# Kernel optimization log

Measured on AMD Instinct MI355X. Metric: run time of the kernel, lower is better.

Reference implementation:

```python
import jax, jax.numpy as jnp
import numpy as np
from jax import lax

T, N, E = 8192, 33, 64
D_IN, D_H, D_LSTM, N_CLS = 3, 64, 128, 5


def _lin(k, out_d, in_d):
    return jax.random.normal(k, (out_d, in_d), jnp.float32) / np.sqrt(in_d)


def setup_inputs() -> dict:
    key = jax.random.key(0)
    ks = jax.random.split(key, 16)
    x = jax.random.normal(ks[0], (T, N, D_IN), jnp.float32)
    edge_src = jax.random.randint(ks[1], (E,), 0, N)
    edge_dst = jax.random.randint(ks[2], (E,), 0, N)
    return {
        "x": x,
        "edge_src": edge_src,
        "edge_dst": edge_dst,
        "W_rel1": _lin(ks[3], D_H, D_IN),
        "b_rel1": jnp.zeros((D_H,), jnp.float32),
        "W_root1": _lin(ks[4], D_H, D_IN),
        "W_rel2": _lin(ks[5], D_H, D_H),
        "b_rel2": jnp.zeros((D_H,), jnp.float32),
        "W_root2": _lin(ks[6], D_H, D_H),
        "W_ih": _lin(ks[7], 4 * D_LSTM, D_H),
        "W_hh": _lin(ks[8], 4 * D_LSTM, D_LSTM),
        "b_ih": jnp.zeros((4 * D_LSTM,), jnp.float32),
        "b_hh": jnp.zeros((4 * D_LSTM,), jnp.float32),
        "W_fc": _lin(ks[9], N_CLS, D_LSTM),
        "b_fc": jnp.zeros((N_CLS,), jnp.float32),
    }


def graph_conv(x, src, dst, W_rel, b_rel, W_root):
    # PyG GraphConv (aggr='add'): lin_rel(scatter_add(x[src] -> dst)) + lin_root(x)
    msg = x[:, src, :]                              # [T, E, d]
    agg = jnp.zeros_like(x).at[:, dst, :].add(msg)  # [T, N, d]
    return agg @ W_rel.T + b_rel + x @ W_root.T     # [T, N, out]


def lstm_last_hidden(seq, W_ih, W_hh, b_ih, b_hh):
    # seq: [T, D_H]; torch gate order i, f, g, o
    def step(carry, xt):
        h, c = carry
        gates = xt @ W_ih.T + h @ W_hh.T + b_ih + b_hh  # [4*D_LSTM]
        i, f, g, o = jnp.split(gates, 4)
        c = jax.nn.sigmoid(f) * c + jax.nn.sigmoid(i) * jnp.tanh(g)
        h = jax.nn.sigmoid(o) * jnp.tanh(c)
        return (h, c), None
    init = (jnp.zeros((D_LSTM,), seq.dtype), jnp.zeros((D_LSTM,), seq.dtype))
    (hT, _), _ = lax.scan(step, init, seq)
    return hT


def reference(x, edge_src, edge_dst, W_rel1, b_rel1, W_root1, W_rel2, b_rel2,
              W_root2, W_ih, W_hh, b_ih, b_hh, W_fc, b_fc):
    h = graph_conv(x, edge_src, edge_dst, W_rel1, b_rel1, W_root1)  # [T,N,64]
    h = graph_conv(h, edge_src, edge_dst, W_rel2, b_rel2, W_root2)  # [T,N,64]
    h = jax.nn.relu(h)
    seq = h.mean(axis=1)                                            # global_mean_pool per frame -> [T,64]
    hT = lstm_last_hidden(seq, W_ih, W_hh, b_ih, b_hh)              # [128]
    return (hT @ W_fc.T + b_fc)[None, :]                            # [1, 5]
```

## Files before the change

### kernel.cpp

```cpp
#include <hip/hip_runtime.h>
#include <hip/hip_fp16.h>

#define T_LEN 8192
#define N_NODES 33
#define N_EDGES 64
#define DIM_IN 3
#define D_H 64
#define D_LSTM 128
#define N_CLS 5
#define TB 4

typedef float v2f __attribute__((ext_vector_type(2)));
typedef float v4f __attribute__((ext_vector_type(4)));

__global__ __launch_bounds__(64, 2) void gnn_proj_kernel(
    const float* __restrict__ x,
    const int*   __restrict__ esrc,
    const int*   __restrict__ edst,
    const float* __restrict__ W_rel1,
    const float* __restrict__ b_rel1,
    const float* __restrict__ W_root1,
    const float* __restrict__ W_rel2,
    const float* __restrict__ b_rel2,
    const float* __restrict__ W_root2,
    const float* __restrict__ W_ih,
    const float* __restrict__ b_ih,
    const float* __restrict__ b_hh,
    float* __restrict__ A)
{
    const int t0 = blockIdx.x * TB;
    const int j  = threadIdx.x;

    __shared__ __align__(16) float x_s[N_NODES][DIM_IN];
    __shared__ __align__(16) float agg1[N_NODES][DIM_IN];
    __shared__ __align__(16) float h1[N_NODES][D_H];
    __shared__ __align__(16) float agg2[N_NODES][D_H];
    __shared__ __align__(16) float seq_s[TB][D_H];
    __shared__ int es[N_EDGES], ed[N_EDGES];

    es[j] = esrc[j];
    ed[j] = edst[j];

    const float wr1_0 = W_rel1[j*3+0], wr1_1 = W_rel1[j*3+1], wr1_2 = W_rel1[j*3+2];
    const float wt1_0 = W_root1[j*3+0], wt1_1 = W_root1[j*3+1], wt1_2 = W_root1[j*3+2];
    const float br1 = b_rel1[j];
    const float br2 = b_rel2[j];

    float wr2[D_H], wt2[D_H];
    #pragma unroll
    for (int k = 0; k < D_H; ++k) {
        wr2[k] = W_rel2[j*D_H + k];
        wt2[k] = W_root2[j*D_H + k];
    }

    for (int tt = 0; tt < TB; ++tt) {
        const int t = t0 + tt;
        __syncthreads();

        const float* xt = x + (size_t)t * (N_NODES * DIM_IN);
        for (int i = j; i < N_NODES * DIM_IN; i += 64) x_s[0][i] = xt[i];
        __syncthreads();

        if (j < N_NODES) {
            float a0 = 0.f, a1 = 0.f, a2 = 0.f;
            for (int e = 0; e < N_EDGES; ++e) {
                if (ed[e] == j) {
                    a0 += x_s[es[e]][0];
                    a1 += x_s[es[e]][1];
                    a2 += x_s[es[e]][2];
                }
            }
            agg1[j][0] = a0; agg1[j][1] = a1; agg1[j][2] = a2;
        }
        __syncthreads();

        for (int n = 0; n < N_NODES; ++n) {
            float v = br1
                + agg1[n][0]*wr1_0 + agg1[n][1]*wr1_1 + agg1[n][2]*wr1_2
                + x_s[n][0]*wt1_0  + x_s[n][1]*wt1_1  + x_s[n][2]*wt1_2;
            h1[n][j]  = v;
            agg2[n][j] = 0.f;
        }
        __syncthreads();

        for (int e = 0; e < N_EDGES; ++e) {
            agg2[ed[e]][j] += h1[es[e]][j];
        }
        __syncthreads();

        float seqv = 0.f;
        for (int n = 0; n < N_NODES; ++n) {
            const float4* ag4 = (const float4*)agg2[n];
            const float4* h4  = (const float4*)h1[n];
            float acc0 = br2, acc1 = 0.f, acc2 = 0.f, acc3 = 0.f;
            #pragma unroll
            for (int k4 = 0; k4 < D_H/4; ++k4) {
                float4 av = ag4[k4];
                float4 hv = h4[k4];
                acc0 += av.x * wr2[4*k4+0] + hv.x * wt2[4*k4+0];
                acc1 += av.y * wr2[4*k4+1] + hv.y * wt2[4*k4+1];
                acc2 += av.z * wr2[4*k4+2] + hv.z * wt2[4*k4+2];
                acc3 += av.w * wr2[4*k4+3] + hv.w * wt2[4*k4+3];
            }
            float acc = (acc0 + acc1) + (acc2 + acc3);
            seqv += fmaxf(acc, 0.f);
        }
        seq_s[tt][j] = seqv * (1.0f / 33.0f);
    }
    __syncthreads();

    #pragma unroll
    for (int m = 0; m < 8; ++m) {
        const int o = m * 64 + j;
        const float bias = b_ih[o] + b_hh[o];
        const float4* w4 = (const float4*)(W_ih + (size_t)o * D_H);
        float acc[TB];
        #pragma unroll
        for (int tt = 0; tt < TB; ++tt) acc[tt] = bias;
        #pragma unroll
        for (int k4 = 0; k4 < D_H/4; ++k4) {
            float4 wv = w4[k4];
            #pragma unroll
            for (int tt = 0; tt < TB; ++tt) {
                const float4* s4 = (const float4*)seq_s[tt];
                float4 sv = s4[k4];
                acc[tt] += sv.x*wv.x + sv.y*wv.y + sv.z*wv.z + sv.w*wv.w;
            }
        }
        #pragma unroll
        for (int tt = 0; tt < TB; ++tt) {
            A[((size_t)(t0 + tt) * 128 + (o & 127)) * 4 + (o >> 7)] = acc[tt];
        }
    }
}


#define CVTPK(D,S0,S1) \
  "v_cvt_f16_f32 v190, v" #S0 "\n\t" \
  "v_cvt_f16_f32 v191, v" #S1 "\n\t" \
  "v_and_b32 v190, 0xffff, v190\n\t" \
  "v_lshlrev_b32 v191, 16, v191\n\t" \
  "v_or_b32 v" #D ", v190, v191\n\t"

#define ROWPACK(D0,D1,D2,D3,D4,D5,D6,D7,D8,D9,D10,D11,D12,D13,D14,D15) \
  CVTPK(D0,128,129) CVTPK(D1,130,131) CVTPK(D2,132,133) CVTPK(D3,134,135) \
  CVTPK(D4,136,137) CVTPK(D5,138,139) CVTPK(D6,140,141) CVTPK(D7,142,143) \
  CVTPK(D8,144,145) CVTPK(D9,146,147) CVTPK(D10,148,149) CVTPK(D11,150,151) \
  CVTPK(D12,152,153) CVTPK(D13,154,155) CVTPK(D14,156,157) CVTPK(D15,158,159)

#define FRAGLOAD(WA) \
  "global_load_dwordx4 v[128:131], %[" #WA "], off\n\t" \
  "global_load_dwordx4 v[132:135], %[" #WA "], off offset:16\n\t" \
  "global_load_dwordx4 v[136:139], %[" #WA "], off offset:128\n\t" \
  "global_load_dwordx4 v[140:143], %[" #WA "], off offset:144\n\t" \
  "global_load_dwordx4 v[144:147], %[" #WA "], off offset:256\n\t" \
  "global_load_dwordx4 v[148:151], %[" #WA "], off offset:272\n\t" \
  "global_load_dwordx4 v[152:155], %[" #WA "], off offset:384\n\t" \
  "global_load_dwordx4 v[156:159], %[" #WA "], off offset:400\n\t" \
  "s_waitcnt vmcnt(0)\n\t"

#define HALF(P0,P3, PC0,PC1,PC2,PC3, R0,R1,R2,R3, WOFF) \
  "ds_read_b128 v[64:67], %[rb] offset:" #R0 "\n\t" \
  "ds_read_b128 v[68:71], %[rb] offset:" #R1 "\n\t" \
  "ds_read_b128 v[72:75], %[rb] offset:" #R2 "\n\t" \
  "ds_read_b128 v[76:79], %[rb] offset:" #R3 "\n\t" \
  "v_add_u32 v189, s80, %[at]\n\t" \
  "global_load_dwordx4 v[" #P0 ":" #P3 "], v189, %[ab]\n\t" \
  "s_add_u32 s80, s80, 2048\n\t" \
  "s_cmp_lg_u32 s80, 0x1000000\n\t" \
  "s_cselect_b32 s80, s80, 0\n\t" \
  "s_waitcnt lgkmcnt(0)\n\t" \
   \
  "v_mfma_f32_16x16x32_f16 v[80:83], v[0:3],   v[64:67], v[164:167]\n\t" \
  "v_mfma_f32_16x16x32_f16 v[84:87], v[16:19], v[64:67], v[164:167]\n\t" \
  "v_mfma_f32_16x16x32_f16 v[88:91], v[32:35], v[64:67], v[164:167]\n\t" \
  "v_mfma_f32_16x16x32_f16 v[92:95], v[48:51], v[64:67], v[164:167]\n\t" \
  "v_mfma_f32_16x16x32_f16 v[80:83], v[4:7],   v[68:71], v[80:83]\n\t" \
  "v_mfma_f32_16x16x32_f16 v[84:87], v[20:23], v[68:71], v[84:87]\n\t" \
  "v_mfma_f32_16x16x32_f16 v[88:91], v[36:39], v[68:71], v[88:91]\n\t" \
  "v_mfma_f32_16x16x32_f16 v[92:95], v[52:55], v[68:71], v[92:95]\n\t" \
  "v_mfma_f32_16x16x32_f16 v[80:83], v[8:11],  v[72:75], v[80:83]\n\t" \
  "v_mfma_f32_16x16x32_f16 v[84:87], v[24:27], v[72:75], v[84:87]\n\t" \
  "v_mfma_f32_16x16x32_f16 v[88:91], v[40:43], v[72:75], v[88:91]\n\t" \
  "v_mfma_f32_16x16x32_f16 v[92:95], v[56:59], v[72:75], v[92:95]\n\t" \
  "v_mfma_f32_16x16x32_f16 v[80:83], v[12:15], v[76:79], v[80:83]\n\t" \
  "v_mfma_f32_16x16x32_f16 v[84:87], v[28:31], v[76:79], v[84:87]\n\t" \
  "v_mfma_f32_16x16x32_f16 v[88:91], v[44:47], v[76:79], v[88:91]\n\t" \
  "v_mfma_f32_16x16x32_f16 v[92:95], v[60:63], v[76:79], v[92:95]\n\t" \
  "s_nop 7\n\t" \
  "s_nop 7\n\t" \
   \
  "v_cndmask_b32 v184, v80, v82, %[sb1]\n\t" \
  "v_cndmask_b32 v185, v81, v83, %[sb1]\n\t" \
  "v_cndmask_b32 v176, v184, v185, %[sb0]\n\t" \
  "v_cndmask_b32 v184, v84, v86, %[sb1]\n\t" \
  "v_cndmask_b32 v185, v85, v87, %[sb1]\n\t" \
  "v_cndmask_b32 v177, v184, v185, %[sb0]\n\t" \
  "v_cndmask_b32 v184, v88, v90, %[sb1]\n\t" \
  "v_cndmask_b32 v185, v89, v91, %[sb1]\n\t" \
  "v_cndmask_b32 v178, v184, v185, %[sb0]\n\t" \
  "v_cndmask_b32 v184, v92, v94, %[sb1]\n\t" \
  "v_cndmask_b32 v185, v93, v95, %[sb1]\n\t" \
  "v_cndmask_b32 v179, v184, v185, %[sb0]\n\t" \
   \
  "s_waitcnt vmcnt(1)\n\t" \
  "v_add_f32 v176, v176, v" #PC0 "\n\t" \
  "v_add_f32 v177, v177, v" #PC1 "\n\t" \
  "v_add_f32 v178, v178, v" #PC2 "\n\t" \
  "v_add_f32 v179, v179, v" #PC3 "\n\t" \
   \
  "v_mul_f32 v180, s87, v176\n\t" \
  "v_mul_f32 v181, s87, v177\n\t" \
  "v_mul_f32 v182, s87, v179\n\t" \
  "v_mul_f32 v183, s88, v178\n\t" \
  "v_exp_f32 v180, v180\n\t" \
  "v_exp_f32 v181, v181\n\t" \
  "v_exp_f32 v182, v182\n\t" \
  "v_exp_f32 v183, v183\n\t" \
  "v_add_f32 v180, 1.0, v180\n\t" \
  "v_add_f32 v181, 1.0, v181\n\t" \
  "v_add_f32 v182, 1.0, v182\n\t" \
  "v_add_f32 v183, 1.0, v183\n\t" \
  "v_rcp_f32 v183, v183\n\t" \
  "v_rcp_f32 v180, v180\n\t" \
  "v_rcp_f32 v181, v181\n\t" \
  "v_rcp_f32 v182, v182\n\t" \
  "v_add_f32 v183, v183, v183\n\t" \
  "v_add_f32 v183, -1.0, v183\n\t" \
  "v_mul_f32 v184, v180, v183\n\t" \
  "v_fma_f32 v190, v181, v190, v184\n\t" \
  "v_mul_f32 v185, s88, v190\n\t" \
  "v_exp_f32 v185, v185\n\t" \
  "s_nop 1\n\t" \
  "v_add_f32 v185, 1.0, v185\n\t" \
  "v_rcp_f32 v185, v185\n\t" \
  "s_nop 1\n\t" \
  "v_fma_f32 v185, v185, 2.0, -1.0\n\t" \
  "v_mul_f32 v188, v182, v185\n\t" \
  "v_cvt_f16_f32 v188, v188\n\t" \
   \
  "s_and_saveexec_b64 s[84:85], s[82:83]\n\t" \
  "ds_write_b16 %[wr], v188 offset:" #WOFF "\n\t" \
  "s_mov_b64 exec, s[84:85]\n\t" \
  "s_waitcnt lgkmcnt(0)\n\t" \
  "s_barrier\n\t"

__global__ __launch_bounds__(512, 2)
__attribute__((amdgpu_waves_per_eu(2, 2)))
void lstm_kernel(
    const float* __restrict__ A,
    const float* __restrict__ W_hh,
    const float* __restrict__ W_fc,
    const float* __restrict__ b_fc,
    float* __restrict__ out)
{
    const int tid  = threadIdx.x;
    const int lane = tid & 63;
    const int wave = tid >> 6;
    const int q0   = wave * 16;
    const int row  = lane & 15;
    const int kb8  = (lane >> 4) * 8;
    const int u    = q0 + 4 * (lane >> 4) + (lane & 3);

    __shared__ __align__(16) float h_s[2][64];

    if (tid < 128) ((float*)h_s)[tid] = 0.f;
    __syncthreads();

    const unsigned long long wai = (unsigned long long)(uintptr_t)(W_hh + (size_t)(q0 + row)        * D_LSTM + kb8);
    const unsigned long long waf = (unsigned long long)(uintptr_t)(W_hh + (size_t)(128 + q0 + row)  * D_LSTM + kb8);
    const unsigned long long wag = (unsigned long long)(uintptr_t)(W_hh + (size_t)(256 + q0 + row)  * D_LSTM + kb8);
    const unsigned long long wao = (unsigned long long)(uintptr_t)(W_hh + (size_t)(384 + q0 + row)  * D_LSTM + kb8);
    const unsigned int atid = (unsigned int)(u * 16);
    const unsigned int lds0 = (unsigned int)(uintptr_t)&h_s[0][0];
    const unsigned int rb   = lds0 + (unsigned int)((lane >> 4) * 16);
    const unsigned int wr   = lds0 + (unsigned int)(u * 2);
    const unsigned long long wm  = __ballot((lane & 12) == 0);
    const unsigned long long sb0 = __ballot(lane & 1);
    const unsigned long long sb1 = __ballot(lane & 2);

    asm volatile(
        "s_mov_b32 s80, 2048\n\t"
        "s_mov_b32 s86, 4096\n\t"
        "s_mov_b32 s87, 0xBFB8AA3B\n\t"
        "s_mov_b32 s88, 0xC038AA3B\n\t"
        "s_mov_b64 s[82:83], %[wm]\n\t"
        FRAGLOAD(wai)
        ROWPACK(0,1,2,3,4,5,6,7,8,9,10,11,12,13,14,15)
        FRAGLOAD(waf)
        ROWPACK(16,17,18,19,20,21,22,23,24,25,26,27,28,29,30,31)
        FRAGLOAD(wag)
        ROWPACK(32,33,34,35,36,37,38,39,40,41,42,43,44,45,46,47)
        FRAGLOAD(wao)
        ROWPACK(48,49,50,51,52,53,54,55,56,57,58,59,60,61,62,63)
        "v_mov_b32 v164, 0\n\t"
        "v_mov_b32 v165, 0\n\t"
        "v_mov_b32 v166, 0\n\t"
        "v_mov_b32 v167, 0\n\t"
        "global_load_dwordx4 v[168:171], %[at], %[ab]\n\t"
        "s_waitcnt vmcnt(0)\n\t"
        "v_mov_b32 v190, 0\n\t"
        "1:\n\t"
        HALF(172,175, 168,169,170,171, 0,64,128,192, 256)
        HALF(168,171, 172,173,174,175, 256,320,384,448, 0)
        "s_sub_u32 s86, s86, 1\n\t"
        "s_cmp_lg_u32 s86, 0\n\t"
        "s_cbranch_scc1 1b\n\t"
        :
        : [wai]"v"(wai), [waf]"v"(waf), [wag]"v"(wag), [wao]"v"(wao),
          [ab]"s"(A), [at]"v"(atid), [rb]"v"(rb), [wr]"v"(wr), [wm]"s"(wm),
          [sb0]"s"(sb0), [sb1]"s"(sb1)
        : "v0","v1","v2","v3","v4","v5","v6","v7","v8","v9",
          "v10","v11","v12","v13","v14","v15","v16","v17","v18","v19",
          "v20","v21","v22","v23","v24","v25","v26","v27","v28","v29",
          "v30","v31","v32","v33","v34","v35","v36","v37","v38","v39",
          "v40","v41","v42","v43","v44","v45","v46","v47","v48","v49",
          "v50","v51","v52","v53","v54","v55","v56","v57","v58","v59",
          "v60","v61","v62","v63","v64","v65","v66","v67","v68","v69",
          "v70","v71","v72","v73","v74","v75","v76","v77","v78","v79",
          "v80","v81","v82","v83","v84","v85","v86","v87","v88","v89",
          "v90","v91","v92","v93","v94","v95","v96","v97","v98","v99",
          "v100","v101","v102","v103","v104","v105","v106","v107","v108","v109",
          "v110","v111","v112","v113","v114","v115","v116","v117","v118","v119",
          "v120","v121","v122","v123","v124","v125","v126","v127","v128","v129",
          "v130","v131","v132","v133","v134","v135","v136","v137","v138","v139",
          "v140","v141","v142","v143","v144","v145","v146","v147","v148","v149",
          "v150","v151","v152","v153","v154","v155","v156","v157","v158","v159",
          "v160","v161","v162","v163","v164","v165","v166","v167","v168","v169",
          "v170","v171","v172","v173","v174","v175","v176","v177","v178","v179",
          "v180","v181","v182","v183","v184","v185","v186","v187","v188","v189",
          "v190","v191",
          "s80","s81","s82","s83","s84","s85","s86","s87","s88",
          "scc","memory"
    );

    __syncthreads();

    if (tid < N_CLS) {
        const __half* hh = (const __half*)&h_s[0][0];
        float acc = b_fc[tid];
        #pragma unroll
        for (int k = 0; k < D_LSTM; ++k) {
            acc += __half2float(hh[k]) * W_fc[tid * D_LSTM + k];
        }
        out[tid] = acc;
    }
}

extern "C" void kernel_launch(void* const* d_in, const int* in_sizes, int n_in,
                              void* d_out, int out_size, void* d_ws, size_t ws_size,
                              hipStream_t stream) {
    const float* x       = (const float*)d_in[0];
    const int*   esrc    = (const int*)  d_in[1];
    const int*   edst    = (const int*)  d_in[2];
    const float* W_rel1  = (const float*)d_in[3];
    const float* b_rel1  = (const float*)d_in[4];
    const float* W_root1 = (const float*)d_in[5];
    const float* W_rel2  = (const float*)d_in[6];
    const float* b_rel2  = (const float*)d_in[7];
    const float* W_root2 = (const float*)d_in[8];
    const float* W_ih    = (const float*)d_in[9];
    const float* W_hh    = (const float*)d_in[10];
    const float* b_ih    = (const float*)d_in[11];
    const float* b_hh    = (const float*)d_in[12];
    const float* W_fc    = (const float*)d_in[13];
    const float* b_fc    = (const float*)d_in[14];

    float* out = (float*)d_out;
    float* A   = (float*)d_ws;

    gnn_proj_kernel<<<T_LEN / TB, 64, 0, stream>>>(
        x, esrc, edst, W_rel1, b_rel1, W_root1,
        W_rel2, b_rel2, W_root2, W_ih, b_ih, b_hh, A);

    lstm_kernel<<<1, 512, 0, stream>>>(A, W_hh, W_fc, b_fc, out);
}
```

Measured before the change: 3.876 ms.

## Halve LSTM workgroup to four waves, each computing two hidden-unit groups

The sequential LSTM kernel now runs with 256 threads (4 waves) instead of 512. Each wave holds twice as many W_hh fragments in registers and issues 32 MFMAs per half-step, computing two hidden units per lane. The aim is to cut barrier and synchronisation cost per timestep by involving fewer waves. The trade-offs are a longer per-wave critical path, since each wave does twice the MFMA and transcendental work, and much higher VGPR use.

```diff
diff --git a/kernel.cpp b/kernel.cpp
--- a/kernel.cpp
+++ b/kernel.cpp
@@ -136,117 +136,176 @@
 
 
 #define CVTPK(D,S0,S1) \
-  "v_cvt_f16_f32 v190, v" #S0 "\n\t" \
-  "v_cvt_f16_f32 v191, v" #S1 "\n\t" \
-  "v_and_b32 v190, 0xffff, v190\n\t" \
-  "v_lshlrev_b32 v191, 16, v191\n\t" \
-  "v_or_b32 v" #D ", v190, v191\n\t"
+  "v_cvt_f16_f32 v204, v" #S0 "\n\t" \
+  "v_cvt_f16_f32 v205, v" #S1 "\n\t" \
+  "v_and_b32 v204, 0xffff, v204\n\t" \
+  "v_lshlrev_b32 v205, 16, v205\n\t" \
+  "v_or_b32 v" #D ", v204, v205\n\t"
 
 #define ROWPACK(D0,D1,D2,D3,D4,D5,D6,D7,D8,D9,D10,D11,D12,D13,D14,D15) \
-  CVTPK(D0,128,129) CVTPK(D1,130,131) CVTPK(D2,132,133) CVTPK(D3,134,135) \
-  CVTPK(D4,136,137) CVTPK(D5,138,139) CVTPK(D6,140,141) CVTPK(D7,142,143) \
-  CVTPK(D8,144,145) CVTPK(D9,146,147) CVTPK(D10,148,149) CVTPK(D11,150,151) \
-  CVTPK(D12,152,153) CVTPK(D13,154,155) CVTPK(D14,156,157) CVTPK(D15,158,159)
-
-#define FRAGLOAD(WA) \
-  "global_load_dwordx4 v[128:131], %[" #WA "], off\n\t" \
-  "global_load_dwordx4 v[132:135], %[" #WA "], off offset:16\n\t" \
-  "global_load_dwordx4 v[136:139], %[" #WA "], off offset:128\n\t" \
-  "global_load_dwordx4 v[140:143], %[" #WA "], off offset:144\n\t" \
-  "global_load_dwordx4 v[144:147], %[" #WA "], off offset:256\n\t" \
-  "global_load_dwordx4 v[148:151], %[" #WA "], off offset:272\n\t" \
-  "global_load_dwordx4 v[152:155], %[" #WA "], off offset:384\n\t" \
-  "global_load_dwordx4 v[156:159], %[" #WA "], off offset:400\n\t" \
+  CVTPK(D0,144,145) CVTPK(D1,146,147) CVTPK(D2,148,149) CVTPK(D3,150,151) \
+  CVTPK(D4,152,153) CVTPK(D5,154,155) CVTPK(D6,156,157) CVTPK(D7,158,159) \
+  CVTPK(D8,160,161) CVTPK(D9,162,163) CVTPK(D10,164,165) CVTPK(D11,166,167) \
+  CVTPK(D12,168,169) CVTPK(D13,170,171) CVTPK(D14,172,173) CVTPK(D15,174,175)
+
+#define FRAGLOAD(VOFF) \
+  "global_load_dwordx4 v[144:147], " VOFF ", %[whh]\n\t" \
+  "global_load_dwordx4 v[148:151], " VOFF ", %[whh] offset:16\n\t" \
+  "global_load_dwordx4 v[152:155], " VOFF ", %[whh] offset:128\n\t" \
+  "global_load_dwordx4 v[156:159], " VOFF ", %[whh] offset:144\n\t" \
+  "global_load_dwordx4 v[160:163], " VOFF ", %[whh] offset:256\n\t" \
+  "global_load_dwordx4 v[164:167], " VOFF ", %[whh] offset:272\n\t" \
+  "global_load_dwordx4 v[168:171], " VOFF ", %[whh] offset:384\n\t" \
+  "global_load_dwordx4 v[172:175], " VOFF ", %[whh] offset:400\n\t" \
   "s_waitcnt vmcnt(0)\n\t"
 
-#define HALF(P0,P3, PC0,PC1,PC2,PC3, R0,R1,R2,R3, WOFF) \
-  "ds_read_b128 v[64:67], %[rb] offset:" #R0 "\n\t" \
-  "ds_read_b128 v[68:71], %[rb] offset:" #R1 "\n\t" \
-  "ds_read_b128 v[72:75], %[rb] offset:" #R2 "\n\t" \
-  "ds_read_b128 v[76:79], %[rb] offset:" #R3 "\n\t" \
-  "v_add_u32 v189, s80, %[at]\n\t" \
-  "global_load_dwordx4 v[" #P0 ":" #P3 "], v189, %[ab]\n\t" \
+#define HALF(P0,P3,P4,P7, PC0,PC1,PC2,PC3,PC4,PC5,PC6,PC7, R0,R1,R2,R3, W1,W2) \
+  "ds_read_b128 v[128:131], %[rb] offset:" #R0 "\n\t" \
+  "ds_read_b128 v[132:135], %[rb] offset:" #R1 "\n\t" \
+  "ds_read_b128 v[136:139], %[rb] offset:" #R2 "\n\t" \
+  "ds_read_b128 v[140:143], %[rb] offset:" #R3 "\n\t" \
+  "v_add_u32 v232, s80, %[at]\n\t" \
+  "global_load_dwordx4 v[" #P0 ":" #P3 "], v232, %[ab]\n\t" \
+  "global_load_dwordx4 v[" #P4 ":" #P7 "], v232, %[ab] offset:256\n\t" \
   "s_add_u32 s80, s80, 2048\n\t" \
   "s_cmp_lg_u32 s80, 0x1000000\n\t" \
   "s_cselect_b32 s80, s80, 0\n\t" \
   "s_waitcnt lgkmcnt(0)\n\t" \
    \
-  "v_mfma_f32_16x16x32_f16 v[80:83], v[0:3],   v[64:67], v[164:167]\n\t" \
-  "v_mfma_f32_16x16x32_f16 v[84:87], v[16:19], v[64:67], v[164:167]\n\t" \
-  "v_mfma_f32_16x16x32_f16 v[88:91], v[32:35], v[64:67], v[164:167]\n\t" \
-  "v_mfma_f32_16x16x32_f16 v[92:95], v[48:51], v[64:67], v[164:167]\n\t" \
-  "v_mfma_f32_16x16x32_f16 v[80:83], v[4:7],   v[68:71], v[80:83]\n\t" \
-  "v_mfma_f32_16x16x32_f16 v[84:87], v[20:23], v[68:71], v[84:87]\n\t" \
-  "v_mfma_f32_16x16x32_f16 v[88:91], v[36:39], v[68:71], v[88:91]\n\t" \
-  "v_mfma_f32_16x16x32_f16 v[92:95], v[52:55], v[68:71], v[92:95]\n\t" \
-  "v_mfma_f32_16x16x32_f16 v[80:83], v[8:11],  v[72:75], v[80:83]\n\t" \
-  "v_mfma_f32_16x16x32_f16 v[84:87], v[24:27], v[72:75], v[84:87]\n\t" \
-  "v_mfma_f32_16x16x32_f16 v[88:91], v[40:43], v[72:75], v[88:91]\n\t" \
-  "v_mfma_f32_16x16x32_f16 v[92:95], v[56:59], v[72:75], v[92:95]\n\t" \
-  "v_mfma_f32_16x16x32_f16 v[80:83], v[12:15], v[76:79], v[80:83]\n\t" \
-  "v_mfma_f32_16x16x32_f16 v[84:87], v[28:31], v[76:79], v[84:87]\n\t" \
-  "v_mfma_f32_16x16x32_f16 v[88:91], v[44:47], v[76:79], v[88:91]\n\t" \
-  "v_mfma_f32_16x16x32_f16 v[92:95], v[60:63], v[76:79], v[92:95]\n\t" \
+  "v_mfma_f32_16x16x32_f16 v[144:147], v[0:3],     v[128:131], v[200:203]\n\t" \
+  "v_mfma_f32_16x16x32_f16 v[148:151], v[16:19],   v[128:131], v[200:203]\n\t" \
+  "v_mfma_f32_16x16x32_f16 v[152:155], v[32:35],   v[128:131], v[200:203]\n\t" \
+  "v_mfma_f32_16x16x32_f16 v[156:159], v[48:51],   v[128:131], v[200:203]\n\t" \
+  "v_mfma_f32_16x16x32_f16 v[160:163], v[64:67],   v[128:131], v[200:203]\n\t" \
+  "v_mfma_f32_16x16x32_f16 v[164:167], v[80:83],   v[128:131], v[200:203]\n\t" \
+  "v_mfma_f32_16x16x32_f16 v[168:171], v[96:99],   v[128:131], v[200:203]\n\t" \
+  "v_mfma_f32_16x16x32_f16 v[172:175], v[112:115], v[128:131], v[200:203]\n\t" \
+  "v_mfma_f32_16x16x32_f16 v[144:147], v[4:7],     v[132:135], v[144:147]\n\t" \
+  "v_mfma_f32_16x16x32_f16 v[148:151], v[20:23],   v[132:135], v[148:151]\n\t" \
+  "v_mfma_f32_16x16x32_f16 v[152:155], v[36:39],   v[132:135], v[152:155]\n\t" \
+  "v_mfma_f32_16x16x32_f16 v[156:159], v[52:55],   v[132:135], v[156:159]\n\t" \
+  "v_mfma_f32_16x16x32_f16 v[160:163], v[68:71],   v[132:135], v[160:163]\n\t" \
+  "v_mfma_f32_16x16x32_f16 v[164:167], v[84:87],   v[132:135], v[164:167]\n\t" \
+  "v_mfma_f32_16x16x32_f16 v[168:171], v[100:103], v[132:135], v[168:171]\n\t" \
+  "v_mfma_f32_16x16x32_f16 v[172:175], v[116:119], v[132:135], v[172:175]\n\t" \
+  "v_mfma_f32_16x16x32_f16 v[144:147], v[8:11],    v[136:139], v[144:147]\n\t" \
+  "v_mfma_f32_16x16x32_f16 v[148:151], v[24:27],   v[136:139], v[148:151]\n\t" \
+  "v_mfma_f32_16x16x32_f16 v[152:155], v[40:43],   v[136:139], v[152:155]\n\t" \
+  "v_mfma_f32_16x16x32_f16 v[156:159], v[56:59],   v[136:139], v[156:159]\n\t" \
+  "v_mfma_f32_16x16x32_f16 v[160:163], v[72:75],   v[136:139], v[160:163]\n\t" \
+  "v_mfma_f32_16x16x32_f16 v[164:167], v[88:91],   v[136:139], v[164:167]\n\t" \
+  "v_mfma_f32_16x16x32_f16 v[168:171], v[104:107], v[136:139], v[168:171]\n\t" \
+  "v_mfma_f32_16x16x32_f16 v[172:175], v[120:123], v[136:139], v[172:175]\n\t" \
+  "v_mfma_f32_16x16x32_f16 v[144:147], v[12:15],   v[140:143], v[144:147]\n\t" \
+  "v_mfma_f32_16x16x32_f16 v[148:151], v[28:31],   v[140:143], v[148:151]\n\t" \
+  "v_mfma_f32_16x16x32_f16 v[152:155], v[44:47],   v[140:143], v[152:155]\n\t" \
+  "v_mfma_f32_16x16x32_f16 v[156:159], v[60:63],   v[140:143], v[156:159]\n\t" \
+  "v_mfma_f32_16x16x32_f16 v[160:163], v[76:79],   v[140:143], v[160:163]\n\t" \
+  "v_mfma_f32_16x16x32_f16 v[164:167], v[92:95],   v[140:143], v[164:167]\n\t" \
+  "v_mfma_f32_16x16x32_f16 v[168:171], v[108:111], v[140:143], v[168:171]\n\t" \
+  "v_mfma_f32_16x16x32_f16 v[172:175], v[124:127], v[140:143], v[172:175]\n\t" \
   "s_nop 7\n\t" \
   "s_nop 7\n\t" \
    \
-  "v_cndmask_b32 v184, v80, v82, %[sb1]\n\t" \
-  "v_cndmask_b32 v185, v81, v83, %[sb1]\n\t" \
-  "v_cndmask_b32 v176, v184, v185, %[sb0]\n\t" \
-  "v_cndmask_b32 v184, v84, v86, %[sb1]\n\t" \
-  "v_cndmask_b32 v185, v85, v87, %[sb1]\n\t" \
-  "v_cndmask_b32 v177, v184, v185, %[sb0]\n\t" \
-  "v_cndmask_b32 v184, v88, v90, %[sb1]\n\t" \
-  "v_cndmask_b32 v185, v89, v91, %[sb1]\n\t" \
-  "v_cndmask_b32 v178, v184, v185, %[sb0]\n\t" \
-  "v_cndmask_b32 v184, v92, v94, %[sb1]\n\t" \
-  "v_cndmask_b32 v185, v93, v95, %[sb1]\n\t" \
-  "v_cndmask_b32 v179, v184, v185, %[sb0]\n\t" \
+  "v_cndmask_b32 v204, v144, v146, %[sb1]\n\t" \
+  "v_cndmask_b32 v205, v145, v147, %[sb1]\n\t" \
+  "v_cndmask_b32 v208, v204, v205, %[sb0]\n\t" \
+  "v_cndmask_b32 v204, v148, v150, %[sb1]\n\t" \
+  "v_cndmask_b32 v205, v149, v151, %[sb1]\n\t" \
+  "v_cndmask_b32 v209, v204, v205, %[sb0]\n\t" \
+  "v_cndmask_b32 v204, v152, v154, %[sb1]\n\t" \
+  "v_cndmask_b32 v205, v153, v155, %[sb1]\n\t" \
+  "v_cndmask_b32 v210, v204, v205, %[sb0]\n\t" \
+  "v_cndmask_b32 v204, v156, v158, %[sb1]\n\t" \
+  "v_cndmask_b32 v205, v157, v159, %[sb1]\n\t" \
+  "v_cndmask_b32 v211, v204, v205, %[sb0]\n\t" \
+  "v_cndmask_b32 v204, v160, v162, %[sb1]\n\t" \
+  "v_cndmask_b32 v205, v161, v163, %[sb1]\n\t" \
+  "v_cndmask_b32 v212, v204, v205, %[sb0]\n\t" \
+  "v_cndmask_b32 v204, v164, v166, %[sb1]\n\t" \
+  "v_cndmask_b32 v205, v165, v167, %[sb1]\n\t" \
+  "v_cndmask_b32 v213, v204, v205, %[sb0]\n\t" \
+  "v_cndmask_b32 v204, v168, v170, %[sb1]\n\t" \
+  "v_cndmask_b32 v205, v169, v171, %[sb1]\n\t" \
+  "v_cndmask_b32 v214, v204, v205, %[sb0]\n\t" \
+  "v_cndmask_b32 v204, v172, v174, %[sb1]\n\t" \
+  "v_cndmask_b32 v205, v173, v175, %[sb1]\n\t" \
+  "v_cndmask_b32 v215, v204, v205, %[sb0]\n\t" \
    \
-  "s_waitcnt vmcnt(1)\n\t" \
-  "v_add_f32 v176, v176, v" #PC0 "\n\t" \
-  "v_add_f32 v177, v177, v" #PC1 "\n\t" \
-  "v_add_f32 v178, v178, v" #PC2 "\n\t" \
-  "v_add_f32 v179, v179, v" #PC3 "\n\t" \
+  "s_waitcnt vmcnt(2)\n\t" \
+  "v_add_f32 v208, v208, v" #PC0 "\n\t" \
+  "v_add_f32 v209, v209, v" #PC1 "\n\t" \
+  "v_add_f32 v210, v210, v" #PC2 "\n\t" \
+  "v_add_f32 v211, v211, v" #PC3 "\n\t" \
+  "v_add_f32 v212, v212, v" #PC4 "\n\t" \
+  "v_add_f32 v213, v213, v" #PC5 "\n\t" \
+  "v_add_f32 v214, v214, v" #PC6 "\n\t" \
+  "v_add_f32 v215, v215, v" #PC7 "\n\t" \
    \
-  "v_mul_f32 v180, s87, v176\n\t" \
-  "v_mul_f32 v181, s87, v177\n\t" \
-  "v_mul_f32 v182, s87, v179\n\t" \
-  "v_mul_f32 v183, s88, v178\n\t" \
-  "v_exp_f32 v180, v180\n\t" \
-  "v_exp_f32 v181, v181\n\t" \
-  "v_exp_f32 v182, v182\n\t" \
-  "v_exp_f32 v183, v183\n\t" \
-  "v_add_f32 v180, 1.0, v180\n\t" \
-  "v_add_f32 v181, 1.0, v181\n\t" \
-  "v_add_f32 v182, 1.0, v182\n\t" \
-  "v_add_f32 v183, 1.0, v183\n\t" \
-  "v_rcp_f32 v183, v183\n\t" \
-  "v_rcp_f32 v180, v180\n\t" \
-  "v_rcp_f32 v181, v181\n\t" \
-  "v_rcp_f32 v182, v182\n\t" \
-  "v_add_f32 v183, v183, v183\n\t" \
-  "v_add_f32 v183, -1.0, v183\n\t" \
-  "v_mul_f32 v184, v180, v183\n\t" \
-  "v_fma_f32 v190, v181, v190, v184\n\t" \
-  "v_mul_f32 v185, s88, v190\n\t" \
-  "v_exp_f32 v185, v185\n\t" \
+  "v_mul_f32 v216, s87, v208\n\t" \
+  "v_mul_f32 v217, s87, v209\n\t" \
+  "v_mul_f32 v218, s88, v210\n\t" \
+  "v_mul_f32 v219, s87, v211\n\t" \
+  "v_mul_f32 v220, s87, v212\n\t" \
+  "v_mul_f32 v221, s87, v213\n\t" \
+  "v_mul_f32 v222, s88, v214\n\t" \
+  "v_mul_f32 v223, s87, v215\n\t" \
+  "v_exp_f32 v216, v216\n\t" \
+  "v_exp_f32 v217, v217\n\t" \
+  "v_exp_f32 v218, v218\n\t" \
+  "v_exp_f32 v219, v219\n\t" \
+  "v_exp_f32 v220, v220\n\t" \
+  "v_exp_f32 v221, v221\n\t" \
+  "v_exp_f32 v222, v222\n\t" \
+  "v_exp_f32 v223, v223\n\t" \
+  "v_add_f32 v216, 1.0, v216\n\t" \
+  "v_add_f32 v217, 1.0, v217\n\t" \
+  "v_add_f32 v218, 1.0, v218\n\t" \
+  "v_add_f32 v219, 1.0, v219\n\t" \
+  "v_add_f32 v220, 1.0, v220\n\t" \
+  "v_add_f32 v221, 1.0, v221\n\t" \
+  "v_add_f32 v222, 1.0, v222\n\t" \
+  "v_add_f32 v223, 1.0, v223\n\t" \
+  "v_rcp_f32 v218, v218\n\t" \
+  "v_rcp_f32 v222, v222\n\t" \
+  "v_rcp_f32 v216, v216\n\t" \
+  "v_rcp_f32 v217, v217\n\t" \
+  "v_rcp_f32 v219, v219\n\t" \
+  "v_rcp_f32 v220, v220\n\t" \
+  "v_rcp_f32 v221, v221\n\t" \
+  "v_rcp_f32 v223, v223\n\t" \
+  "v_fma_f32 v218, v218, 2.0, -1.0\n\t" \
+  "v_fma_f32 v222, v222, 2.0, -1.0\n\t" \
+  "v_mul_f32 v224, v216, v218\n\t" \
+  "v_mul_f32 v225, v220, v222\n\t" \
+  "v_fma_f32 v228, v217, v228, v224\n\t" \
+  "v_fma_f32 v229, v221, v229, v225\n\t" \
+  "v_mul_f32 v226, s88, v228\n\t" \
+  "v_mul_f32 v227, s88, v229\n\t" \
+  "v_exp_f32 v226, v226\n\t" \
+  "v_exp_f32 v227, v227\n\t" \
   "s_nop 1\n\t" \
-  "v_add_f32 v185, 1.0, v185\n\t" \
-  "v_rcp_f32 v185, v185\n\t" \
+  "v_add_f32 v226, 1.0, v226\n\t" \
+  "v_add_f32 v227, 1.0, v227\n\t" \
+  "v_rcp_f32 v226, v226\n\t" \
+  "v_rcp_f32 v227, v227\n\t" \
   "s_nop 1\n\t" \
-  "v_fma_f32 v185, v185, 2.0, -1.0\n\t" \
-  "v_mul_f32 v188, v182, v185\n\t" \
-  "v_cvt_f16_f32 v188, v188\n\t" \
+  "v_fma_f32 v226, v226, 2.0, -1.0\n\t" \
+  "v_fma_f32 v227, v227, 2.0, -1.0\n\t" \
+  "v_mul_f32 v230, v219, v226\n\t" \
+  "v_mul_f32 v231, v223, v227\n\t" \
+  "v_cvt_f16_f32 v230, v230\n\t" \
+  "v_cvt_f16_f32 v231, v231\n\t" \
    \
   "s_and_saveexec_b64 s[84:85], s[82:83]\n\t" \
-  "ds_write_b16 %[wr], v188 offset:" #WOFF "\n\t" \
+  "ds_write_b16 %[wr], v230 offset:" #W1 "\n\t" \
+  "ds_write_b16 %[wr], v231 offset:" #W2 "\n\t" \
   "s_mov_b64 exec, s[84:85]\n\t" \
   "s_waitcnt lgkmcnt(0)\n\t" \
   "s_barrier\n\t"
 
-__global__ __launch_bounds__(512, 2)
-__attribute__((amdgpu_waves_per_eu(2, 2)))
+__global__ __launch_bounds__(256, 1)
+__attribute__((amdgpu_waves_per_eu(1, 1)))
 void lstm_kernel(
     const float* __restrict__ A,
     const float* __restrict__ W_hh,
@@ -257,24 +316,21 @@
     const int tid  = threadIdx.x;
     const int lane = tid & 63;
     const int wave = tid >> 6;
-    const int q0   = wave * 16;
+    const int q0   = wave * 32;
     const int row  = lane & 15;
     const int kb8  = (lane >> 4) * 8;
-    const int u    = q0 + 4 * (lane >> 4) + (lane & 3);
+    const int u1   = q0 + 4 * (lane >> 4) + (lane & 3);
 
     __shared__ __align__(16) float h_s[2][64];
 
     if (tid < 128) ((float*)h_s)[tid] = 0.f;
     __syncthreads();
 
-    const unsigned long long wai = (unsigned long long)(uintptr_t)(W_hh + (size_t)(q0 + row)        * D_LSTM + kb8);
-    const unsigned long long waf = (unsigned long long)(uintptr_t)(W_hh + (size_t)(128 + q0 + row)  * D_LSTM + kb8);
-    const unsigned long long wag = (unsigned long long)(uintptr_t)(W_hh + (size_t)(256 + q0 + row)  * D_LSTM + kb8);
-    const unsigned long long wao = (unsigned long long)(uintptr_t)(W_hh + (size_t)(384 + q0 + row)  * D_LSTM + kb8);
-    const unsigned int atid = (unsigned int)(u * 16);
+    const unsigned int wo = (unsigned int)(((q0 + row) * D_LSTM + kb8) * 4);
+    const unsigned int atid = (unsigned int)(u1 * 16);
     const unsigned int lds0 = (unsigned int)(uintptr_t)&h_s[0][0];
     const unsigned int rb   = lds0 + (unsigned int)((lane >> 4) * 16);
-    const unsigned int wr   = lds0 + (unsigned int)(u * 2);
+    const unsigned int wr   = lds0 + (unsigned int)(u1 * 2);
     const unsigned long long wm  = __ballot((lane & 12) == 0);
     const unsigned long long sb0 = __ballot(lane & 1);
     const unsigned long long sb1 = __ballot(lane & 2);
@@ -285,31 +341,47 @@
         "s_mov_b32 s87, 0xBFB8AA3B\n\t"
         "s_mov_b32 s88, 0xC038AA3B\n\t"
         "s_mov_b64 s[82:83], %[wm]\n\t"
-        FRAGLOAD(wai)
+        FRAGLOAD("%[wo]")
         ROWPACK(0,1,2,3,4,5,6,7,8,9,10,11,12,13,14,15)
-        FRAGLOAD(waf)
+        "v_add_u32 v232, 0x10000, %[wo]\n\t"
+        FRAGLOAD("v232")
         ROWPACK(16,17,18,19,20,21,22,23,24,25,26,27,28,29,30,31)
-        FRAGLOAD(wag)
+        "v_add_u32 v232, 0x20000, %[wo]\n\t"
+        FRAGLOAD("v232")
         ROWPACK(32,33,34,35,36,37,38,39,40,41,42,43,44,45,46,47)
-        FRAGLOAD(wao)
+        "v_add_u32 v232, 0x30000, %[wo]\n\t"
+        FRAGLOAD("v232")
         ROWPACK(48,49,50,51,52,53,54,55,56,57,58,59,60,61,62,63)
-        "v_mov_b32 v164, 0\n\t"
-        "v_mov_b32 v165, 0\n\t"
-        "v_mov_b32 v166, 0\n\t"
-        "v_mov_b32 v167, 0\n\t"
-        "global_load_dwordx4 v[168:171], %[at], %[ab]\n\t"
+        "v_add_u32 v232, 0x2000, %[wo]\n\t"
+        FRAGLOAD("v232")
+        ROWPACK(64,65,66,67,68,69,70,71,72,73,74,75,76,77,78,79)
+        "v_add_u32 v232, 0x12000, %[wo]\n\t"
+        FRAGLOAD("v232")
+        ROWPACK(80,81,82,83,84,85,86,87,88,89,90,91,92,93,94,95)
+        "v_add_u32 v232, 0x22000, %[wo]\n\t"
+        FRAGLOAD("v232")
+        ROWPACK(96,97,98,99,100,101,102,103,104,105,106,107,108,109,110,111)
+        "v_add_u32 v232, 0x32000, %[wo]\n\t"
+        FRAGLOAD("v232")
+        ROWPACK(112,113,114,115,116,117,118,119,120,121,122,123,124,125,126,127)
+        "v_mov_b32 v200, 0\n\t"
+        "v_mov_b32 v201, 0\n\t"
+        "v_mov_b32 v202, 0\n\t"
+        "v_mov_b32 v203, 0\n\t"
+        "v_mov_b32 v228, 0\n\t"
+        "v_mov_b32 v229, 0\n\t"
+        "global_load_dwordx4 v[176:179], %[at], %[ab]\n\t"
+        "global_load_dwordx4 v[180:183], %[at], %[ab] offset:256\n\t"
         "s_waitcnt vmcnt(0)\n\t"
-        "v_mov_b32 v190, 0\n\t"
         "1:\n\t"
-        HALF(172,175, 168,169,170,171, 0,64,128,192, 256)
-        HALF(168,171, 172,173,174,175, 256,320,384,448, 0)
+        HALF(184,187,188,191, 176,177,178,179,180,181,182,183, 0,64,128,192, 256,288)
+        HALF(176,179,180,183, 184,185,186,187,188,189,190,191, 256,320,384,448, 0,32)
         "s_sub_u32 s86, s86, 1\n\t"
         "s_cmp_lg_u32 s86, 0\n\t"
         "s_cbranch_scc1 1b\n\t"
         :
-        : [wai]"v"(wai), [waf]"v"(waf), [wag]"v"(wag), [wao]"v"(wao),
-          [ab]"s"(A), [at]"v"(atid), [rb]"v"(rb), [wr]"v"(wr), [wm]"s"(wm),
-          [sb0]"s"(sb0), [sb1]"s"(sb1)
+        : [whh]"s"(W_hh), [wo]"v"(wo), [ab]"s"(A), [at]"v"(atid),
+          [rb]"v"(rb), [wr]"v"(wr), [wm]"s"(wm), [sb0]"s"(sb0), [sb1]"s"(sb1)
         : "v0","v1","v2","v3","v4","v5","v6","v7","v8","v9",
           "v10","v11","v12","v13","v14","v15","v16","v17","v18","v19",
           "v20","v21","v22","v23","v24","v25","v26","v27","v28","v29",
@@ -329,7 +401,11 @@
           "v160","v161","v162","v163","v164","v165","v166","v167","v168","v169",
           "v170","v171","v172","v173","v174","v175","v176","v177","v178","v179",
           "v180","v181","v182","v183","v184","v185","v186","v187","v188","v189",
-          "v190","v191",
+          "v190","v191","v192","v193","v194","v195","v196","v197","v198","v199",
+          "v200","v201","v202","v203","v204","v205","v206","v207","v208","v209",
+          "v210","v211","v212","v213","v214","v215","v216","v217","v218","v219",
+          "v220","v221","v222","v223","v224","v225","v226","v227","v228","v229",
+          "v230","v231","v232","v233","v234","v235",
           "s80","s81","s82","s83","s84","s85","s86","s87","s88",
           "scc","memory"
     );
@@ -373,5 +449,5 @@
         x, esrc, edst, W_rel1, b_rel1, W_root1,
         W_rel2, b_rel2, W_root2, W_ih, b_ih, b_hh, A);
 
-    lstm_kernel<<<1, 512, 0, stream>>>(A, W_hh, W_fc, b_fc, out);
+    lstm_kernel<<<1, 256, 0, stream>>>(A, W_hh, W_fc, b_fc, out);
 }
```

Result: slower. 4.911 ms (+26.7%).

## Spread LSTM gate activations across lanes and gather with DPP row rotates

Applied to the files above, without the earlier changes.

Each lane now computes a single gate activation (sigmoid, or tanh for the g gate via per-lane scale and offset constants) instead of all four gates redundantly. The pre-activation input load drops to one dword per lane, and the activated i/f/g/o values are gathered to every lane with DPP row_ror moves before the cell update. This shortens the serial transcendental chain on the recurrent critical path, at the cost of extra cndmask selects and DPP moves with their hazard nops.

```diff
diff --git a/kernel.cpp b/kernel.cpp
--- a/kernel.cpp
+++ b/kernel.cpp
@@ -159,13 +159,13 @@
   "global_load_dwordx4 v[156:159], %[" #WA "], off offset:400\n\t" \
   "s_waitcnt vmcnt(0)\n\t"
 
-#define HALF(P0,P3, PC0,PC1,PC2,PC3, R0,R1,R2,R3, WOFF) \
+#define HALF(P, PC, R0,R1,R2,R3, WOFF) \
   "ds_read_b128 v[64:67], %[rb] offset:" #R0 "\n\t" \
   "ds_read_b128 v[68:71], %[rb] offset:" #R1 "\n\t" \
   "ds_read_b128 v[72:75], %[rb] offset:" #R2 "\n\t" \
   "ds_read_b128 v[76:79], %[rb] offset:" #R3 "\n\t" \
   "v_add_u32 v189, s80, %[at]\n\t" \
-  "global_load_dwordx4 v[" #P0 ":" #P3 "], v189, %[ab]\n\t" \
+  "global_load_dword v" #P ", v189, %[ab]\n\t" \
   "s_add_u32 s80, s80, 2048\n\t" \
   "s_cmp_lg_u32 s80, 0x1000000\n\t" \
   "s_cselect_b32 s80, s80, 0\n\t" \
@@ -203,40 +203,39 @@
   "v_cndmask_b32 v185, v93, v95, %[sb1]\n\t" \
   "v_cndmask_b32 v179, v184, v185, %[sb0]\n\t" \
    \
+  "v_cndmask_b32 v180, v176, v177, %[sb2]\n\t" \
+  "v_cndmask_b32 v181, v178, v179, %[sb2]\n\t" \
+  "v_cndmask_b32 v182, v180, v181, %[sb3]\n\t" \
+   \
   "s_waitcnt vmcnt(1)\n\t" \
-  "v_add_f32 v176, v176, v" #PC0 "\n\t" \
-  "v_add_f32 v177, v177, v" #PC1 "\n\t" \
-  "v_add_f32 v178, v178, v" #PC2 "\n\t" \
-  "v_add_f32 v179, v179, v" #PC3 "\n\t" \
-   \
-  "v_mul_f32 v180, s87, v176\n\t" \
-  "v_mul_f32 v181, s87, v177\n\t" \
-  "v_mul_f32 v182, s87, v179\n\t" \
-  "v_mul_f32 v183, s88, v178\n\t" \
-  "v_exp_f32 v180, v180\n\t" \
-  "v_exp_f32 v181, v181\n\t" \
-  "v_exp_f32 v182, v182\n\t" \
+  "v_add_f32 v182, v182, v" #PC "\n\t" \
+   \
+  "v_mul_f32 v183, %[m1], v182\n\t" \
   "v_exp_f32 v183, v183\n\t" \
-  "v_add_f32 v180, 1.0, v180\n\t" \
-  "v_add_f32 v181, 1.0, v181\n\t" \
-  "v_add_f32 v182, 1.0, v182\n\t" \
+  "s_nop 1\n\t" \
   "v_add_f32 v183, 1.0, v183\n\t" \
   "v_rcp_f32 v183, v183\n\t" \
-  "v_rcp_f32 v180, v180\n\t" \
-  "v_rcp_f32 v181, v181\n\t" \
-  "v_rcp_f32 v182, v182\n\t" \
-  "v_add_f32 v183, v183, v183\n\t" \
-  "v_add_f32 v183, -1.0, v183\n\t" \
-  "v_mul_f32 v184, v180, v183\n\t" \
-  "v_fma_f32 v190, v181, v190, v184\n\t" \
-  "v_mul_f32 v185, s88, v190\n\t" \
-  "v_exp_f32 v185, v185\n\t" \
-  "s_nop 1\n\t" \
-  "v_add_f32 v185, 1.0, v185\n\t" \
-  "v_rcp_f32 v185, v185\n\t" \
-  "s_nop 1\n\t" \
-  "v_fma_f32 v185, v185, 2.0, -1.0\n\t" \
-  "v_mul_f32 v188, v182, v185\n\t" \
+  "s_nop 1\n\t" \
+  "v_fma_f32 v183, v183, %[sc], %[ad]\n\t" \
+  "s_nop 1\n\t" \
+   \
+   \
+   \
+  "v_mov_b32_dpp v184, v183 row_ror:4 row_mask:0xf bank_mask:0xf\n\t" \
+  "v_mov_b32_dpp v185, v183 row_ror:8 row_mask:0xf bank_mask:0xf\n\t" \
+  "v_mov_b32_dpp v186, v183 row_ror:12 row_mask:0xf bank_mask:0xf\n\t" \
+   \
+  "v_mul_f32 v187, v183, v185\n\t" \
+  "v_fma_f32 v190, v186, v190, v187\n\t" \
+   \
+  "v_mul_f32 v188, s88, v190\n\t" \
+  "v_exp_f32 v188, v188\n\t" \
+  "s_nop 1\n\t" \
+  "v_add_f32 v188, 1.0, v188\n\t" \
+  "v_rcp_f32 v188, v188\n\t" \
+  "s_nop 1\n\t" \
+  "v_fma_f32 v188, v188, 2.0, -1.0\n\t" \
+  "v_mul_f32 v188, v184, v188\n\t" \
   "v_cvt_f16_f32 v188, v188\n\t" \
    \
   "s_and_saveexec_b64 s[84:85], s[82:83]\n\t" \
@@ -261,6 +260,7 @@
     const int row  = lane & 15;
     const int kb8  = (lane >> 4) * 8;
     const int u    = q0 + 4 * (lane >> 4) + (lane & 3);
+    const int rr   = (lane >> 2) & 3;
 
     __shared__ __align__(16) float h_s[2][64];
 
@@ -271,18 +271,23 @@
     const unsigned long long waf = (unsigned long long)(uintptr_t)(W_hh + (size_t)(128 + q0 + row)  * D_LSTM + kb8);
     const unsigned long long wag = (unsigned long long)(uintptr_t)(W_hh + (size_t)(256 + q0 + row)  * D_LSTM + kb8);
     const unsigned long long wao = (unsigned long long)(uintptr_t)(W_hh + (size_t)(384 + q0 + row)  * D_LSTM + kb8);
-    const unsigned int atid = (unsigned int)(u * 16);
+    const unsigned int atid = (unsigned int)(u * 16 + rr * 4);
     const unsigned int lds0 = (unsigned int)(uintptr_t)&h_s[0][0];
     const unsigned int rb   = lds0 + (unsigned int)((lane >> 4) * 16);
     const unsigned int wr   = lds0 + (unsigned int)(u * 2);
     const unsigned long long wm  = __ballot((lane & 12) == 0);
     const unsigned long long sb0 = __ballot(lane & 1);
     const unsigned long long sb1 = __ballot(lane & 2);
+    const unsigned long long sb2 = __ballot(lane & 4);
+    const unsigned long long sb3 = __ballot(lane & 8);
+    const float m1 = (rr == 2) ? -2.8853900817779268f
+                               : -1.4426950408889634f;
+    const float sc = (rr == 2) ? 2.0f : 1.0f;
+    const float ad = (rr == 2) ? -1.0f : 0.0f;
 
     asm volatile(
         "s_mov_b32 s80, 2048\n\t"
         "s_mov_b32 s86, 4096\n\t"
-        "s_mov_b32 s87, 0xBFB8AA3B\n\t"
         "s_mov_b32 s88, 0xC038AA3B\n\t"
         "s_mov_b64 s[82:83], %[wm]\n\t"
         FRAGLOAD(wai)
@@ -297,19 +302,20 @@
         "v_mov_b32 v165, 0\n\t"
         "v_mov_b32 v166, 0\n\t"
         "v_mov_b32 v167, 0\n\t"
-        "global_load_dwordx4 v[168:171], %[at], %[ab]\n\t"
+        "global_load_dword v168, %[at], %[ab]\n\t"
         "s_waitcnt vmcnt(0)\n\t"
         "v_mov_b32 v190, 0\n\t"
         "1:\n\t"
-        HALF(172,175, 168,169,170,171, 0,64,128,192, 256)
-        HALF(168,171, 172,173,174,175, 256,320,384,448, 0)
+        HALF(172, 168, 0,64,128,192, 256)
+        HALF(168, 172, 256,320,384,448, 0)
         "s_sub_u32 s86, s86, 1\n\t"
         "s_cmp_lg_u32 s86, 0\n\t"
         "s_cbranch_scc1 1b\n\t"
         :
         : [wai]"v"(wai), [waf]"v"(waf), [wag]"v"(wag), [wao]"v"(wao),
           [ab]"s"(A), [at]"v"(atid), [rb]"v"(rb), [wr]"v"(wr), [wm]"s"(wm),
-          [sb0]"s"(sb0), [sb1]"s"(sb1)
+          [sb0]"s"(sb0), [sb1]"s"(sb1), [sb2]"s"(sb2), [sb3]"s"(sb3),
+          [m1]"v"(m1), [sc]"v"(sc), [ad]"v"(ad)
         : "v0","v1","v2","v3","v4","v5","v6","v7","v8","v9",
           "v10","v11","v12","v13","v14","v15","v16","v17","v18","v19",
           "v20","v21","v22","v23","v24","v25","v26","v27","v28","v29",
```

Result: faster. 3.731 ms (-3.7%).
